# Optimization experiments

Hardware: AMD Instinct MI355X
Metric: run time of the kernel (lower is better)

Reference implementation:

```python
import jax, jax.numpy as jnp
import numpy as np

SEQ, D_IN, D_OUT = 8192, 1024, 1024

def setup_inputs() -> dict:
    key = jax.random.key(0)
    kx, kq, kk, kv = jax.random.split(key, 4)
    x = jax.random.normal(kx, (SEQ, D_IN), dtype=jnp.float32)
    # original uses torch.rand (uniform [0,1)) for parameters
    W_query = jax.random.uniform(kq, (D_IN, D_OUT), dtype=jnp.float32)
    W_key = jax.random.uniform(kk, (D_IN, D_OUT), dtype=jnp.float32)
    W_value = jax.random.uniform(kv, (D_IN, D_OUT), dtype=jnp.float32)
    return {"x": x, "W_query": W_query, "W_key": W_key, "W_value": W_value}

def reference(x, W_query, W_key, W_value):
    # x: [S, d_in]; projections: [S, d_out]
    queries = x @ W_query
    keys = x @ W_key
    values = x @ W_value
    scale = 1.0 / jnp.sqrt(jnp.asarray(keys.shape[-1], dtype=x.dtype))
    attn_scores = jnp.einsum('sd,td->st', queries, keys) * scale  # [S, S]
    attn_weights = jax.nn.softmax(attn_scores, axis=-1)
    context_vec = attn_weights @ values  # [S, d_out]
    return context_vec
```

## Files before the change

### kernel.cpp

```cpp
#include <hip/hip_runtime.h>
#include <hip/hip_bf16.h>
#include <hip/hip_fp16.h>

#define SEQ 8192
#define DM  1024

typedef __attribute__((ext_vector_type(8))) short    bf16x8;
typedef __attribute__((ext_vector_type(8))) _Float16 f16x8;
typedef __attribute__((ext_vector_type(4))) float    f32x4;

union H8 { _Float16 h[8]; int4 v; };

__device__ __forceinline__ unsigned short f2bf(float f) {
    union { float f; unsigned u; } x; x.f = f;
    unsigned r = x.u + 0x7fffu + ((x.u >> 16) & 1u);
    return (unsigned short)(r >> 16);
}
__device__ __forceinline__ float bf2f(unsigned short h) {
    union { unsigned u; float f; } x; x.u = ((unsigned)h) << 16;
    return x.f;
}

__device__ __forceinline__ void gld16(const unsigned short* g, unsigned short* l) {
    __builtin_amdgcn_global_load_lds(
        (const __attribute__((address_space(1))) void*)g,
        (__attribute__((address_space(3))) void*)l, 16, 0, 0);
}

__global__ __launch_bounds__(256) void prep_kernel(const float* __restrict__ x,
    unsigned short* __restrict__ xhi, unsigned short* __restrict__ xlo,
    float* __restrict__ rsum,
    const float* W0, const float* W1, const float* W2,
    unsigned short* Wqh, unsigned short* Wql,
    unsigned short* Wkh, unsigned short* Wkl,
    unsigned short* H2, unsigned short* L2)
{
    __shared__ float tile[64][65];
    __shared__ float rbuf[4];
    int t = threadIdx.x;

    if (blockIdx.x < 8192) {
        int base = blockIdx.x * 1024 + t * 4;
        float4 v = *(const float4*)(x + base);
        float f[4] = {v.x, v.y, v.z, v.w};
        unsigned short h[4], l[4];
#pragma unroll
        for (int j = 0; j < 4; j++) { h[j] = f2bf(f[j]); l[j] = f2bf(f[j] - bf2f(h[j])); }
        ushort4 hv = {h[0], h[1], h[2], h[3]};
        ushort4 lv = {l[0], l[1], l[2], l[3]};
        *(ushort4*)(xhi + base) = hv;
        *(ushort4*)(xlo + base) = lv;
        float s4 = f[0] + f[1] + f[2] + f[3];
#pragma unroll
        for (int sh = 1; sh < 64; sh <<= 1) s4 += __shfl_xor(s4, sh);
        if ((t & 63) == 0) rbuf[t >> 6] = s4;
        __syncthreads();
        if (t == 0) rsum[blockIdx.x] = rbuf[0] + rbuf[1] + rbuf[2] + rbuf[3];
        return;
    }

    if (blockIdx.x < 8192 + 2048) {
        int id = blockIdx.x - 8192;
        const float* W = (id < 1024) ? W0 : W1;
        unsigned short* H = (id < 1024) ? Wqh : Wkh;
        unsigned short* L = (id < 1024) ? Wql : Wkl;
        int base = (id & 1023) * 1024 + t * 4;
        float4 v = *(const float4*)(W + base);
        float f[4] = {v.x, v.y, v.z, v.w};
        unsigned short h[4], l[4];
#pragma unroll
        for (int j = 0; j < 4; j++) { h[j] = f2bf(f[j]); l[j] = f2bf(f[j] - bf2f(h[j])); }
        ushort4 hv = {h[0], h[1], h[2], h[3]};
        ushort4 lv = {l[0], l[1], l[2], l[3]};
        *(ushort4*)(H + base) = hv;
        *(ushort4*)(L + base) = lv;
        return;
    }

    int id2 = blockIdx.x - 10240;
    int bn = (id2 & 15) * 64;
    int bk = (id2 >> 4) * 64;
    const float* W = W2;

#pragma unroll
    for (int p = 0; p < 4; p++) {
        int r = p * 16 + (t >> 4);
        int c = (t & 15) * 4;
        float4 v = *(const float4*)(W + (size_t)(bk + r) * DM + bn + c);
        tile[r][c] = v.x; tile[r][c+1] = v.y; tile[r][c+2] = v.z; tile[r][c+3] = v.w;
    }
    __syncthreads();
#pragma unroll
    for (int p = 0; p < 2; p++) {
        int task = p * 256 + t;
        int rn = task >> 3;
        int kc = (task & 7) * 8;
        union { unsigned short u[8]; int4 v; } hh, ll;
#pragma unroll
        for (int j = 0; j < 8; j++) {
            float f = tile[kc + j][rn];
            hh.u[j] = f2bf(f);
            ll.u[j] = f2bf(f - bf2f(hh.u[j]));
        }
        size_t o = (size_t)(bn + rn) * DM + bk + kc;
        *(int4*)(H2 + o) = hh.v;
        *(int4*)(L2 + o) = ll.v;
    }
}

template<int MODE, int KD>
__global__ __launch_bounds__(256, 2) void gemm128(
    const unsigned short* A,   const unsigned short* Alo,
    const unsigned short* B_,  const unsigned short* Blo_,
    unsigned short* Chi, unsigned short* Clo,
    _Float16* Cf16, float* Cf32, const float* __restrict__ Scp)
{
    constexpr bool SPLIT = (MODE == 0 || MODE == 5);
    constexpr int NT = (MODE == 5) ? 4 : KD / 32;
    __shared__ alignas(16) unsigned short sAhi[2][128 * 32];
    __shared__ alignas(16) unsigned short sBhi[2][128 * 32];
    __shared__ alignas(16) unsigned short sAlo[SPLIT ? 2 * 128 * 32 : 16];
    __shared__ alignas(16) unsigned short sBlo[SPLIT ? 2 * 128 * 32 : 16];
    __shared__ alignas(16) _Float16 sSc[(MODE == 3) ? 128 * 130 : 8];

    const unsigned short* B   = B_;
    const unsigned short* Blo = Blo_;

    const int m0 = blockIdx.x * 128;
    const int n0 = blockIdx.y * 128;
    const int kbase = (MODE == 5) ? (int)blockIdx.z * 128 : 0;
    const int t = threadIdx.x;
    const int wave = t >> 6, lane = t & 63;
    const int wr = wave >> 1, wc = wave & 1;
    const int i16 = lane & 15, quad = lane >> 4;

    const int rs = wave * 32 + (lane >> 2);
    const int scol = ((lane & 3) ^ ((lane >> 3) & 3)) << 3;
    const size_t aoff = (size_t)(m0 + rs) * KD + scol;
    const size_t boff = (size_t)(n0 + rs) * KD + scol;
    const int ldsb = wave * 1024;

    int offA[4], offB[4];
#pragma unroll
    for (int mt = 0; mt < 4; mt++) {
        int row = wr * 64 + mt * 16 + i16;
        offA[mt] = row * 32 + ((quad ^ ((row >> 1) & 3)) << 3);
    }
#pragma unroll
    for (int nt = 0; nt < 4; nt++) {
        int row = wc * 64 + nt * 16 + i16;
        offB[nt] = row * 32 + ((quad ^ ((row >> 1) & 3)) << 3);
    }

    if constexpr (MODE == 3) {
#pragma unroll
        for (int i = 0; i < 16; i++) {
            int idx = i * 1024 + t * 4;
            int row = idx >> 7, col = idx & 127;
            float4 v = *(const float4*)(Scp + (size_t)(m0 + row) * 128 + col);
            _Float16* d = sSc + row * 130 + col;
            d[0] = (_Float16)v.x; d[1] = (_Float16)v.y;
            d[2] = (_Float16)v.z; d[3] = (_Float16)v.w;
        }
    }

    auto STAGE = [&](int buf, int k) {
        gld16(A + aoff + k,           sAhi[buf] + ldsb);
        gld16(A + aoff + 16 * KD + k, sAhi[buf] + ldsb + 512);
        gld16(B + boff + k,           sBhi[buf] + ldsb);
        gld16(B + boff + 16 * KD + k, sBhi[buf] + ldsb + 512);
        if constexpr (SPLIT) {
            gld16(Alo + aoff + k,           sAlo + buf * 4096 + ldsb);
            gld16(Alo + aoff + 16 * KD + k, sAlo + buf * 4096 + ldsb + 512);
            gld16(Blo + boff + k,           sBlo + buf * 4096 + ldsb);
            gld16(Blo + boff + 16 * KD + k, sBlo + buf * 4096 + ldsb + 512);
        }
    };

    f32x4 acc[4][4] = {};

    STAGE(0, kbase);
    __syncthreads();

    for (int kt = 0; kt < NT; ++kt) {
        const int cur = kt & 1;
        const int k = kbase + kt * 32;

        bf16x8 ahi[4], alo[4], bhi[4], blo[4];
#pragma unroll
        for (int mt = 0; mt < 4; mt++) {
            ahi[mt] = *(const bf16x8*)(sAhi[cur] + offA[mt]);
            if constexpr (SPLIT) alo[mt] = *(const bf16x8*)(sAlo + cur * 4096 + offA[mt]);
        }
#pragma unroll
        for (int nt = 0; nt < 4; nt++) {
            bhi[nt] = *(const bf16x8*)(sBhi[cur] + offB[nt]);
            if constexpr (SPLIT) blo[nt] = *(const bf16x8*)(sBlo + cur * 4096 + offB[nt]);
        }
        if constexpr (MODE == 3) {
#pragma unroll
            for (int mt = 0; mt < 4; mt++) {
                _Float16 sc = sSc[(wr * 64 + mt * 16 + i16) * 130 + (k >> 6)];
                f16x8 av = __builtin_bit_cast(f16x8, ahi[mt]);
                av = av * sc;
                ahi[mt] = __builtin_bit_cast(bf16x8, av);
            }
        }

        if (kt + 1 < NT) STAGE(cur ^ 1, k + 32);

        __builtin_amdgcn_s_setprio(1);
#pragma unroll
        for (int nt = 0; nt < 4; nt++)
#pragma unroll
            for (int mt = 0; mt < 4; mt++) {
                if constexpr (MODE == 3) {
                    acc[mt][nt] = __builtin_amdgcn_mfma_f32_16x16x32_f16(
                        __builtin_bit_cast(f16x8, ahi[mt]), __builtin_bit_cast(f16x8, bhi[nt]),
                        acc[mt][nt], 0, 0, 0);
                } else {
                    acc[mt][nt] = __builtin_amdgcn_mfma_f32_16x16x32_bf16(ahi[mt], bhi[nt], acc[mt][nt], 0, 0, 0);
                    if constexpr (SPLIT) {
                        acc[mt][nt] = __builtin_amdgcn_mfma_f32_16x16x32_bf16(ahi[mt], blo[nt], acc[mt][nt], 0, 0, 0);
                        acc[mt][nt] = __builtin_amdgcn_mfma_f32_16x16x32_bf16(alo[mt], bhi[nt], acc[mt][nt], 0, 0, 0);
                    }
                }
            }
        __builtin_amdgcn_s_setprio(0);

        asm volatile("s_waitcnt vmcnt(0)" ::: "memory");
        __builtin_amdgcn_s_barrier();
        __builtin_amdgcn_sched_barrier(0);
    }

    if constexpr (MODE == 0) {
#pragma unroll
        for (int mt = 0; mt < 4; mt++)
#pragma unroll
            for (int nt = 0; nt < 4; nt++)
#pragma unroll
                for (int r = 0; r < 4; r++) {
                    int row = m0 + wr * 64 + mt * 16 + quad * 4 + r;
                    int col = n0 + wc * 64 + nt * 16 + i16;
                    float v = acc[mt][nt][r];
                    unsigned short h = f2bf(v);
                    Chi[(size_t)row * DM + col] = h;
                    Clo[(size_t)row * DM + col] = f2bf(v - bf2f(h));
                }
    } else if constexpr (MODE == 1) {
#pragma unroll
        for (int mt = 0; mt < 4; mt++)
#pragma unroll
            for (int nt = 0; nt < 4; nt++) {
                int row0 = m0 + wr * 64 + mt * 16 + quad * 4;
                int col  = n0 + wc * 64 + nt * 16 + i16;
                union { _Float16 h[4]; unsigned long long q; } p;
#pragma unroll
                for (int r = 0; r < 4; r++) p.h[r] = (_Float16)acc[mt][nt][r];
                *(unsigned long long*)(Cf16 + (size_t)col * SEQ + row0) = p.q;
            }
    } else if constexpr (MODE == 5) {
        float* Gp = Cf32 + ((size_t)blockIdx.z << 20);
#pragma unroll
        for (int mt = 0; mt < 4; mt++)
#pragma unroll
            for (int nt = 0; nt < 4; nt++) {
                int row0 = m0 + wr * 64 + mt * 16 + quad * 4;
                int col  = n0 + wc * 64 + nt * 16 + i16;
                union { float f[4]; float4 v; } p;
#pragma unroll
                for (int r = 0; r < 4; r++) p.f[r] = acc[mt][nt][r];
                *(float4*)(Gp + (size_t)col * DM + row0) = p.v;
            }
    } else {
#pragma unroll
        for (int mt = 0; mt < 4; mt++)
#pragma unroll
            for (int nt = 0; nt < 4; nt++)
#pragma unroll
                for (int r = 0; r < 4; r++) {
                    int row = m0 + wr * 64 + mt * 16 + quad * 4 + r;
                    int col = n0 + wc * 64 + nt * 16 + i16;
                    Cf32[(size_t)row * DM + col] = acc[mt][nt][r];
                }
    }
}

__global__ __launch_bounds__(256) void greduce(const float* __restrict__ Gp,
    unsigned short* __restrict__ Ghi, unsigned short* __restrict__ Glo)
{
    int e = blockIdx.x;
    int d0 = threadIdx.x * 4;
    float s[4] = {0.f, 0.f, 0.f, 0.f};
#pragma unroll
    for (int z = 0; z < 8; z++) {
        float4 v = *(const float4*)(Gp + ((size_t)z << 20) + (size_t)e * DM + d0);
        s[0] += v.x; s[1] += v.y; s[2] += v.z; s[3] += v.w;
    }
    unsigned short h[4], l[4];
#pragma unroll
    for (int j = 0; j < 4; j++) {
        float f = s[j] - 256.0f;
        h[j] = f2bf(f);
        l[j] = f2bf(f - bf2f(h[j]));
    }
    ushort4 hv = {h[0], h[1], h[2], h[3]};
    ushort4 lv = {l[0], l[1], l[2], l[3]};
    *(ushort4*)(Ghi + (size_t)e * DM + d0) = hv;
    *(ushort4*)(Glo + (size_t)e * DM + d0) = lv;
}

__global__ __launch_bounds__(1024) void scores256(
    const unsigned short* __restrict__ Yh, const unsigned short* __restrict__ Yl,
    const unsigned short* __restrict__ Xh, const unsigned short* __restrict__ Xl,
    const float* __restrict__ rsum,
    _Float16* __restrict__ Eo, float* __restrict__ Tt, float* __restrict__ Zt)
{
    constexpr int KD = 1024;
    constexpr int NT = KD / 32;
    __shared__ alignas(16) unsigned short lds[2 * 4 * 8192];
    __shared__ float srM[256], srN[256];

    const int flat = blockIdx.y * gridDim.x + blockIdx.x;
    const int wg = (flat & 7) * 128 + (flat >> 3);
    const int m0 = (wg >> 5) << 8;
    const int n0 = (wg & 31) << 8;

    const int t = threadIdx.x;
    const int wave = t >> 6, lane = t & 63;
    const int wr = wave >> 2, wc = wave & 3;
    const int i16 = lane & 15, quad = lane >> 4;

    if (t < 256) srM[t] = rsum[m0 + t];
    else if (t < 512) srN[t - 256] = rsum[n0 + t - 256];

    const int srow = wave * 16 + (lane >> 2);
    const int scol = ((lane & 3) ^ ((lane >> 3) & 3)) << 3;
    const size_t ga = (size_t)(m0 + srow) * KD + scol;
    const size_t gb = (size_t)(n0 + srow) * KD + scol;
    const int ldw = wave * 512;

    int offA[4], offB[4];
#pragma unroll
    for (int mt = 0; mt < 4; mt++) {
        int row = wr * 64 + mt * 16 + i16;
        offA[mt] = row * 32 + ((quad ^ ((row >> 1) & 3)) << 3);
    }
#pragma unroll
    for (int nt = 0; nt < 4; nt++) {
        int row = wc * 64 + nt * 16 + i16;
        offB[nt] = row * 32 + ((quad ^ ((row >> 1) & 3)) << 3);
    }

    f32x4 acc[4][4] = {};

    auto STAGE = [&](int buf, int kt) {
        unsigned short* p = lds + buf * 32768;
        const int k = kt * 32;
        gld16(Yh + ga + k, p + ldw);
        gld16(Yl + ga + k, p + 8192  + ldw);
        gld16(Xh + gb + k, p + 16384 + ldw);
        gld16(Xl + gb + k, p + 24576 + ldw);
    };

    STAGE(0, 0);
    asm volatile("s_waitcnt vmcnt(0)" ::: "memory");
    __builtin_amdgcn_s_barrier();
    __builtin_amdgcn_sched_barrier(0);

    for (int kt = 0; kt < NT; ++kt) {
        const int cur = kt & 1;
        const unsigned short* pAh = lds + cur * 32768;
        const unsigned short* pAl = pAh + 8192;
        const unsigned short* pBh = pAh + 16384;
        const unsigned short* pBl = pAh + 24576;

        bf16x8 bh[4], bl[4];
#pragma unroll
        for (int ni = 0; ni < 4; ni++) {
            bh[ni] = *(const bf16x8*)(pBh + offB[ni]);
            bl[ni] = *(const bf16x8*)(pBl + offB[ni]);
        }
        if (kt + 1 < NT) STAGE(cur ^ 1, kt + 1);

        __builtin_amdgcn_s_setprio(1);
#pragma unroll
        for (int mi = 0; mi < 4; mi++) {
            bf16x8 ah = *(const bf16x8*)(pAh + offA[mi]);
            bf16x8 al = *(const bf16x8*)(pAl + offA[mi]);
#pragma unroll
            for (int ni = 0; ni < 4; ni++) {
                f32x4 c = acc[mi][ni];
                c = __builtin_amdgcn_mfma_f32_16x16x32_bf16(ah, bh[ni], c, 0, 0, 0);
                c = __builtin_amdgcn_mfma_f32_16x16x32_bf16(ah, bl[ni], c, 0, 0, 0);
                c = __builtin_amdgcn_mfma_f32_16x16x32_bf16(al, bh[ni], c, 0, 0, 0);
                acc[mi][ni] = c;
            }
        }
        __builtin_amdgcn_s_setprio(0);

        asm volatile("s_waitcnt vmcnt(0)" ::: "memory");
        __builtin_amdgcn_s_barrier();
        __builtin_amdgcn_sched_barrier(0);
    }

    const float scale = 0.03125f;
    const float RC = 8.0f;
    const int tix = (n0 + wc * 64) >> 6;
    const float rn0 = RC * srN[wc * 64 + i16];
    const float rn1 = RC * srN[wc * 64 + 16 + i16];
    const float rn2 = RC * srN[wc * 64 + 32 + i16];
    const float rn3 = RC * srN[wc * 64 + 48 + i16];
#pragma unroll
    for (int mt = 0; mt < 4; mt++)
#pragma unroll
        for (int r = 0; r < 4; r++) {
            float rm = srM[wr * 64 + mt * 16 + quad * 4 + r];
            float s0 = acc[mt][0][r] * scale + rm * rn0;
            float s1 = acc[mt][1][r] * scale + rm * rn1;
            float s2 = acc[mt][2][r] * scale + rm * rn2;
            float s3 = acc[mt][3][r] * scale + rm * rn3;
            float mx = fmaxf(fmaxf(s0, s1), fmaxf(s2, s3));
            mx = fmaxf(mx, __shfl_xor(mx, 1));
            mx = fmaxf(mx, __shfl_xor(mx, 2));
            mx = fmaxf(mx, __shfl_xor(mx, 4));
            mx = fmaxf(mx, __shfl_xor(mx, 8));
            float e0 = __expf(s0 - mx), e1 = __expf(s1 - mx);
            float e2 = __expf(s2 - mx), e3 = __expf(s3 - mx);
            float z = e0 + e1 + e2 + e3;
            z += __shfl_xor(z, 1);
            z += __shfl_xor(z, 2);
            z += __shfl_xor(z, 4);
            z += __shfl_xor(z, 8);
            int row = m0 + wr * 64 + mt * 16 + quad * 4 + r;
            if (i16 == 0) {
                Tt[(size_t)row * 128 + tix] = mx;
                Zt[(size_t)row * 128 + tix] = z;
            }
            size_t eb = (size_t)row * SEQ + n0 + wc * 64 + i16;
            Eo[eb +  0] = (_Float16)e0;
            Eo[eb + 16] = (_Float16)e1;
            Eo[eb + 32] = (_Float16)e2;
            Eo[eb + 48] = (_Float16)e3;
        }
}

__global__ __launch_bounds__(256) void sc_reduce(const float* __restrict__ Tt,
    const float* __restrict__ Zt, float* __restrict__ Sc)
{
    int row = blockIdx.x * 4 + (threadIdx.x >> 6);
    int lane = threadIdx.x & 63;
    size_t b = (size_t)row * 128 + lane;
    float t0 = Tt[b], t1 = Tt[b + 64];
    float z0 = Zt[b], z1 = Zt[b + 64];
    float m = fmaxf(t0, t1);
    for (int sh = 1; sh < 64; sh <<= 1) m = fmaxf(m, __shfl_xor(m, sh));
    float l = z0 * __expf(t0 - m) + z1 * __expf(t1 - m);
    for (int sh = 1; sh < 64; sh <<= 1) l += __shfl_xor(l, sh);
    float inv = 1.0f / l;
    Sc[b]      = __expf(t0 - m) * inv;
    Sc[b + 64] = __expf(t1 - m) * inv;
}

extern "C" void kernel_launch(void* const* d_in, const int* in_sizes, int n_in,
                              void* d_out, int out_size, void* d_ws, size_t ws_size,
                              hipStream_t stream)
{
    const float* x  = (const float*)d_in[0];
    const float* Wq = (const float*)d_in[1];
    const float* Wk = (const float*)d_in[2];
    const float* Wv = (const float*)d_in[3];
    float* Out = (float*)d_out;
    char* ws = (char*)d_ws;

    const size_t MB = 1024 * 1024;
    unsigned short* Wqh  = (unsigned short*)(ws + 0 * MB);
    unsigned short* Wql  = (unsigned short*)(ws + 2 * MB);
    unsigned short* Wkh  = (unsigned short*)(ws + 4 * MB);
    unsigned short* Wkl  = (unsigned short*)(ws + 6 * MB);
    unsigned short* Wvth = (unsigned short*)(ws + 8 * MB);
    unsigned short* Wvtl = (unsigned short*)(ws + 10 * MB);
    unsigned short* Ghi  = (unsigned short*)(ws + 12 * MB);
    unsigned short* Glo  = (unsigned short*)(ws + 14 * MB);
    float*          Gp   = (float*)        (ws + 16 * MB);
    _Float16*       E    = (_Float16*)     (ws + 0 * MB);

    size_t off = 128 * MB;
    unsigned short* Yhi = (unsigned short*)(ws + off); off += 16 * MB;
    unsigned short* Ylo = (unsigned short*)(ws + off); off += 16 * MB;
    unsigned short* xhi = (unsigned short*)(ws + off); off += 16 * MB;
    unsigned short* xlo = (unsigned short*)(ws + off); off += 16 * MB;
    _Float16*       Vt  = (_Float16*)      (ws + off); off += 16 * MB;
    float*          Tt  = (float*)         (ws + off); off += (size_t)SEQ * 128 * 4;
    float*          Zt  = (float*)         (ws + off); off += (size_t)SEQ * 128 * 4;
    float*          Sc  = (float*)         (ws + off); off += (size_t)SEQ * 128 * 4;
    float*          rs  = (float*)         (ws + off); off += (size_t)SEQ * 4;

    prep_kernel<<<8192 + 2048 + 256, 256, 0, stream>>>(x, xhi, xlo, rs, Wq, Wk, Wv,
        Wqh, Wql, Wkh, Wkl, Wvth, Wvtl);
    gemm128<5, DM><<<dim3(8, 8, 8), 256, 0, stream>>>(
        Wqh, Wql, Wkh, Wkl, nullptr, nullptr, nullptr, Gp, nullptr);
    greduce<<<1024, 256, 0, stream>>>(Gp, Ghi, Glo);
    gemm128<1, DM><<<dim3(SEQ / 128, DM / 128), 256, 0, stream>>>(
        xhi, nullptr, Wvth, nullptr, nullptr, nullptr, (_Float16*)Vt, nullptr, nullptr);
    gemm128<0, DM><<<dim3(SEQ / 128, DM / 128), 256, 0, stream>>>(
        xhi, xlo, Ghi, Glo, Yhi, Ylo, nullptr, nullptr, nullptr);
    scores256<<<dim3(SEQ / 256, SEQ / 256), 1024, 0, stream>>>(
        Yhi, Ylo, xhi, xlo, rs, E, Tt, Zt);
    sc_reduce<<<SEQ / 4, 256, 0, stream>>>(Tt, Zt, Sc);
    gemm128<3, SEQ><<<dim3(SEQ / 128, DM / 128), 256, 0, stream>>>(
        (const unsigned short*)E, nullptr, (const unsigned short*)Vt, nullptr,
        nullptr, nullptr, nullptr, Out, Sc);
}
```

Before: 687.6 us.

## Switch score GEMM to fp16 split with single-term x operand

The scores kernel now stores the Y projection as an fp16 hi/lo pair and x as a single fp16 tensor. This cuts the split-precision product from three bf16 MFMAs to two f16 MFMAs per tile and drops one of the four LDS staging streams. The cost is a lower-precision x operand and fp16 range limits on Y, plus an extra x conversion written during prep. Memory traffic in the main scores loop falls by a quarter.

```diff
diff --git a/kernel.cpp b/kernel.cpp
--- a/kernel.cpp
+++ b/kernel.cpp
@@ -29,6 +29,7 @@
 
 __global__ __launch_bounds__(256) void prep_kernel(const float* __restrict__ x,
     unsigned short* __restrict__ xhi, unsigned short* __restrict__ xlo,
+    _Float16* __restrict__ xf,
     float* __restrict__ rsum,
     const float* W0, const float* W1, const float* W2,
     unsigned short* Wqh, unsigned short* Wql,
@@ -44,12 +45,17 @@
         float4 v = *(const float4*)(x + base);
         float f[4] = {v.x, v.y, v.z, v.w};
         unsigned short h[4], l[4];
-#pragma unroll
-        for (int j = 0; j < 4; j++) { h[j] = f2bf(f[j]); l[j] = f2bf(f[j] - bf2f(h[j])); }
+        union { _Float16 h4[4]; unsigned long long q; } xq;
+#pragma unroll
+        for (int j = 0; j < 4; j++) {
+            h[j] = f2bf(f[j]); l[j] = f2bf(f[j] - bf2f(h[j]));
+            xq.h4[j] = (_Float16)f[j];
+        }
         ushort4 hv = {h[0], h[1], h[2], h[3]};
         ushort4 lv = {l[0], l[1], l[2], l[3]};
         *(ushort4*)(xhi + base) = hv;
         *(ushort4*)(xlo + base) = lv;
+        *(unsigned long long*)(xf + base) = xq.q;
         float s4 = f[0] + f[1] + f[2] + f[3];
 #pragma unroll
         for (int sh = 1; sh < 64; sh <<= 1) s4 += __shfl_xor(s4, sh);
@@ -243,9 +249,10 @@
                     int row = m0 + wr * 64 + mt * 16 + quad * 4 + r;
                     int col = n0 + wc * 64 + nt * 16 + i16;
                     float v = acc[mt][nt][r];
-                    unsigned short h = f2bf(v);
-                    Chi[(size_t)row * DM + col] = h;
-                    Clo[(size_t)row * DM + col] = f2bf(v - bf2f(h));
+                    _Float16 hv = (_Float16)v;
+                    _Float16 lv = (_Float16)(v - (float)hv);
+                    Chi[(size_t)row * DM + col] = __builtin_bit_cast(unsigned short, hv);
+                    Clo[(size_t)row * DM + col] = __builtin_bit_cast(unsigned short, lv);
                 }
     } else if constexpr (MODE == 1) {
 #pragma unroll
@@ -312,13 +319,13 @@
 
 __global__ __launch_bounds__(1024) void scores256(
     const unsigned short* __restrict__ Yh, const unsigned short* __restrict__ Yl,
-    const unsigned short* __restrict__ Xh, const unsigned short* __restrict__ Xl,
+    const unsigned short* __restrict__ Xf,
     const float* __restrict__ rsum,
     _Float16* __restrict__ Eo, float* __restrict__ Tt, float* __restrict__ Zt)
 {
     constexpr int KD = 1024;
     constexpr int NT = KD / 32;
-    __shared__ alignas(16) unsigned short lds[2 * 4 * 8192];
+    __shared__ alignas(16) unsigned short lds[2 * 3 * 8192];
     __shared__ float srM[256], srN[256];
 
     const int flat = blockIdx.y * gridDim.x + blockIdx.x;
@@ -355,12 +362,11 @@
     f32x4 acc[4][4] = {};
 
     auto STAGE = [&](int buf, int kt) {
-        unsigned short* p = lds + buf * 32768;
+        unsigned short* p = lds + buf * 24576;
         const int k = kt * 32;
         gld16(Yh + ga + k, p + ldw);
         gld16(Yl + ga + k, p + 8192  + ldw);
-        gld16(Xh + gb + k, p + 16384 + ldw);
-        gld16(Xl + gb + k, p + 24576 + ldw);
+        gld16(Xf + gb + k, p + 16384 + ldw);
     };
 
     STAGE(0, 0);
@@ -370,17 +376,14 @@
 
     for (int kt = 0; kt < NT; ++kt) {
         const int cur = kt & 1;
-        const unsigned short* pAh = lds + cur * 32768;
+        const unsigned short* pAh = lds + cur * 24576;
         const unsigned short* pAl = pAh + 8192;
-        const unsigned short* pBh = pAh + 16384;
-        const unsigned short* pBl = pAh + 24576;
-
-        bf16x8 bh[4], bl[4];
-#pragma unroll
-        for (int ni = 0; ni < 4; ni++) {
-            bh[ni] = *(const bf16x8*)(pBh + offB[ni]);
-            bl[ni] = *(const bf16x8*)(pBl + offB[ni]);
-        }
+        const unsigned short* pBf = pAh + 16384;
+
+        bf16x8 bf[4];
+#pragma unroll
+        for (int ni = 0; ni < 4; ni++)
+            bf[ni] = *(const bf16x8*)(pBf + offB[ni]);
         if (kt + 1 < NT) STAGE(cur ^ 1, kt + 1);
 
         __builtin_amdgcn_s_setprio(1);
@@ -391,9 +394,10 @@
 #pragma unroll
             for (int ni = 0; ni < 4; ni++) {
                 f32x4 c = acc[mi][ni];
-                c = __builtin_amdgcn_mfma_f32_16x16x32_bf16(ah, bh[ni], c, 0, 0, 0);
-                c = __builtin_amdgcn_mfma_f32_16x16x32_bf16(ah, bl[ni], c, 0, 0, 0);
-                c = __builtin_amdgcn_mfma_f32_16x16x32_bf16(al, bh[ni], c, 0, 0, 0);
+                c = __builtin_amdgcn_mfma_f32_16x16x32_f16(
+                    __builtin_bit_cast(f16x8, ah), __builtin_bit_cast(f16x8, bf[ni]), c, 0, 0, 0);
+                c = __builtin_amdgcn_mfma_f32_16x16x32_f16(
+                    __builtin_bit_cast(f16x8, al), __builtin_bit_cast(f16x8, bf[ni]), c, 0, 0, 0);
                 acc[mi][ni] = c;
             }
         }
@@ -490,13 +494,14 @@
     unsigned short* Ylo = (unsigned short*)(ws + off); off += 16 * MB;
     unsigned short* xhi = (unsigned short*)(ws + off); off += 16 * MB;
     unsigned short* xlo = (unsigned short*)(ws + off); off += 16 * MB;
+    _Float16*       xf  = (_Float16*)      (ws + off); off += 16 * MB;
     _Float16*       Vt  = (_Float16*)      (ws + off); off += 16 * MB;
     float*          Tt  = (float*)         (ws + off); off += (size_t)SEQ * 128 * 4;
     float*          Zt  = (float*)         (ws + off); off += (size_t)SEQ * 128 * 4;
     float*          Sc  = (float*)         (ws + off); off += (size_t)SEQ * 128 * 4;
     float*          rs  = (float*)         (ws + off); off += (size_t)SEQ * 4;
 
-    prep_kernel<<<8192 + 2048 + 256, 256, 0, stream>>>(x, xhi, xlo, rs, Wq, Wk, Wv,
+    prep_kernel<<<8192 + 2048 + 256, 256, 0, stream>>>(x, xhi, xlo, xf, rs, Wq, Wk, Wv,
         Wqh, Wql, Wkh, Wkl, Wvth, Wvtl);
     gemm128<5, DM><<<dim3(8, 8, 8), 256, 0, stream>>>(
         Wqh, Wql, Wkh, Wkl, nullptr, nullptr, nullptr, Gp, nullptr);
@@ -506,7 +511,7 @@
     gemm128<0, DM><<<dim3(SEQ / 128, DM / 128), 256, 0, stream>>>(
         xhi, xlo, Ghi, Glo, Yhi, Ylo, nullptr, nullptr, nullptr);
     scores256<<<dim3(SEQ / 256, SEQ / 256), 1024, 0, stream>>>(
-        Yhi, Ylo, xhi, xlo, rs, E, Tt, Zt);
+        Yhi, Ylo, (const unsigned short*)xf, rs, E, Tt, Zt);
     sc_reduce<<<SEQ / 4, 256, 0, stream>>>(Tt, Zt, Sc);
     gemm128<3, SEQ><<<dim3(SEQ / 128, DM / 128), 256, 0, stream>>>(
         (const unsigned short*)E, nullptr, (const unsigned short*)Vt, nullptr,
```

After: 632.2 us. 8.1% less time.
